# Performance work log

Hardware: AMD Instinct MI355X
Metric: run time of the kernel (lower is better)

Reference implementation:

```python
import jax, jax.numpy as jnp
import numpy as np

NUM_POSITIONS = 4096
EMBED_DIM = 512
BSZ, SEQ_LEN = 16, 4096


def setup_inputs() -> dict:
    key = jax.random.key(0)
    k1, k2 = jax.random.split(key)
    input_tensor = jax.random.normal(k1, (BSZ, SEQ_LEN, EMBED_DIM), dtype=jnp.float32)
    pv = jax.random.normal(k2, (NUM_POSITIONS, EMBED_DIM), dtype=jnp.float32)
    # L2-normalize each position vector (as in _init_position_vectors)
    pv = pv / jnp.linalg.norm(pv, axis=1, keepdims=True)
    return {"input_tensor": input_tensor, "position_vectors": pv}


def reference(input_tensor, position_vectors):
    # input_tensor: [B, S, D]; position_vectors: [P, D] with S <= P.
    seq_len, d = input_tensor.shape[1], input_tensor.shape[-1]
    pos = position_vectors[:seq_len]  # [S, D]
    # Batched circular convolution over the last axis via rFFT.
    x_fft = jnp.fft.rfft(input_tensor, axis=-1)          # [B, S, D//2+1] complex
    p_fft = jnp.fft.rfft(pos, axis=-1)[None, :, :]       # [1, S, D//2+1]
    out = jnp.fft.irfft(x_fft * p_fft, n=d, axis=-1)     # [B, S, D]
    return out.astype(input_tensor.dtype)
```

## Files before the change

kernel.cpp:

```cpp
#include <hip/hip_runtime.h>
#include <math.h>

#ifndef M_PI
#define M_PI 3.14159265358979323846
#endif

#define BSZ 16
#define SEQ 4096
#define DIM 512

#define REG_SZ 656

__device__ __forceinline__ float2 cadd(float2 a, float2 b){ return make_float2(a.x+b.x, a.y+b.y); }
__device__ __forceinline__ float2 csub(float2 a, float2 b){ return make_float2(a.x-b.x, a.y-b.y); }
__device__ __forceinline__ float2 cmul(float2 a, float2 b){
  return make_float2(fmaf(a.x, b.x, -(a.y*b.y)), fmaf(a.x, b.y, a.y*b.x));
}
__device__ __forceinline__ float2 cmulc(float2 a, float2 b){
  return make_float2(fmaf(a.x, b.x, a.y*b.y), fmaf(a.y, b.x, -(a.x*b.y)));
}
__device__ __forceinline__ float2 mul_mi(float2 a){ return make_float2(a.y, -a.x); }

__device__ __forceinline__ void dft8(const float2* in, float2* out){
  float2 t0 = cadd(in[0], in[4]), t1 = csub(in[0], in[4]);
  float2 t2 = cadd(in[2], in[6]), t3 = csub(in[2], in[6]);
  float2 E0 = cadd(t0, t2), E2 = csub(t0, t2);
  float2 m3 = mul_mi(t3);
  float2 E1 = cadd(t1, m3), E3 = csub(t1, m3);
  float2 s0 = cadd(in[1], in[5]), s1 = csub(in[1], in[5]);
  float2 s2 = cadd(in[3], in[7]), s3 = csub(in[3], in[7]);
  float2 O0 = cadd(s0, s2), O2 = csub(s0, s2);
  float2 n3 = mul_mi(s3);
  float2 O1 = cadd(s1, n3), O3 = csub(s1, n3);
  const float C = 0.70710678118654752440f;
  float2 w1o = make_float2(C*(O1.x + O1.y), C*(O1.y - O1.x));
  float2 w2o = mul_mi(O2);
  float2 w3o = make_float2(C*(O3.y - O3.x), -(C*(O3.x + O3.y)));
  out[0] = cadd(E0, O0); out[4] = csub(E0, O0);
  out[1] = cadd(E1, w1o); out[5] = csub(E1, w1o);
  out[2] = cadd(E2, w2o); out[6] = csub(E2, w2o);
  out[3] = cadd(E3, w3o); out[7] = csub(E3, w3o);
}

__device__ __forceinline__ void idft8(const float2* in, float2* out){
  float2 t[8];
  dft8(in, t);
  out[0]=t[0]; out[1]=t[7]; out[2]=t[6]; out[3]=t[5];
  out[4]=t[4]; out[5]=t[3]; out[6]=t[2]; out[7]=t[1];
}

__device__ __forceinline__ void fft512_fwd(float2* v, float2* lds, int lane,
                                           const float2* wA, const float2* wB){
  const int a = lane >> 3, b = lane & 7;
  float2 t[8];
  dft8(v, t);
  #pragma unroll
  for (int r = 1; r < 8; ++r) t[r] = cmul(t[r], wA[r]);
  __syncthreads();
  #pragma unroll
  for (int r = 0; r < 8; ++r) lds[72*r + lane] = t[r];
  __syncthreads();
  #pragma unroll
  for (int j2 = 0; j2 < 8; ++j2) v[j2] = lds[72*a + b + 8*j2];
  dft8(v, t);
  #pragma unroll
  for (int r2 = 1; r2 < 8; ++r2) t[r2] = cmul(t[r2], wB[r2]);
  __syncthreads();
  #pragma unroll
  for (int r2 = 0; r2 < 8; ++r2) lds[a + 82*r2 + 10*b] = t[r2];
  __syncthreads();
  #pragma unroll
  for (int i2 = 0; i2 < 8; ++i2) v[i2] = lds[a + 82*b + 10*i2];
  dft8(v, t);
  #pragma unroll
  for (int m = 0; m < 8; ++m) v[m] = t[m];
}

__device__ __forceinline__ void fft512_inv(float2* v, float2* lds, int lane,
                                           const float2* wA, const float2* wB){
  const int a = lane >> 3, b = lane & 7;
  float2 t[8];
  idft8(v, t);
  __syncthreads();
  #pragma unroll
  for (int i2 = 0; i2 < 8; ++i2) lds[a + 82*b + 10*i2] = t[i2];
  __syncthreads();
  #pragma unroll
  for (int r2 = 0; r2 < 8; ++r2) v[r2] = lds[a + 82*r2 + 10*b];
  #pragma unroll
  for (int r2 = 1; r2 < 8; ++r2) v[r2] = cmulc(v[r2], wB[r2]);
  idft8(v, t);
  __syncthreads();
  #pragma unroll
  for (int j2 = 0; j2 < 8; ++j2) lds[72*a + b + 8*j2] = t[j2];
  __syncthreads();
  #pragma unroll
  for (int r = 0; r < 8; ++r) v[r] = lds[72*r + lane];
  #pragma unroll
  for (int r = 1; r < 8; ++r) v[r] = cmulc(v[r], wA[r]);
  idft8(v, t);
  #pragma unroll
  for (int j = 0; j < 8; ++j) v[j] = t[j];
}

__global__ void __launch_bounds__(256)
circconv_kernel(const float* __restrict__ x, const float* __restrict__ p,
                float* __restrict__ out){
  __shared__ float2 lds_all[4 * REG_SZ];
  const int lane = threadIdx.x & 63;
  const int wid  = threadIdx.x >> 6;
  float2* lds = lds_all + wid * REG_SZ;

  const int g    = blockIdx.x * 4 + wid;
  const int s    = g >> 1;
  const int half = g & 1;
  const int b    = lane & 7;

  float2 wA[8], wB[8];
  wA[0] = make_float2(1.f, 0.f); wB[0] = make_float2(1.f, 0.f);
  #pragma unroll
  for (int r = 1; r < 8; ++r){
    float sv, cv;
    sincosf(-2.0f*(float)M_PI*(float)(lane*r)*(1.0f/512.0f), &sv, &cv);
    wA[r] = make_float2(cv, sv);
    sincosf(-2.0f*(float)M_PI*(float)(b*r)*(1.0f/64.0f), &sv, &cv);
    wB[r] = make_float2(cv, sv);
  }

  float2 pf[8];
  {
    const float* prow = p + (size_t)s * DIM;
    #pragma unroll
    for (int j = 0; j < 8; ++j) pf[j] = make_float2(prow[lane + 64*j], 0.f);
    fft512_fwd(pf, lds, lane, wA, wB);
    #pragma unroll
    for (int m = 0; m < 8; ++m){ pf[m].x *= (1.0f/512.0f); pf[m].y *= (1.0f/512.0f); }
  }

  const int b_lo = half * 8;
  for (int bb = b_lo; bb < b_lo + 8; bb += 2){
    const size_t base0 = ((size_t)bb       * SEQ + s) * DIM;
    const size_t base1 = ((size_t)(bb + 1) * SEQ + s) * DIM;
    float2 v[8];
    #pragma unroll
    for (int j = 0; j < 8; ++j)
      v[j] = make_float2(x[base0 + lane + 64*j], x[base1 + lane + 64*j]);
    fft512_fwd(v, lds, lane, wA, wB);
    #pragma unroll
    for (int m = 0; m < 8; ++m) v[m] = cmul(v[m], pf[m]);
    fft512_inv(v, lds, lane, wA, wB);
    #pragma unroll
    for (int j = 0; j < 8; ++j){
      out[base0 + lane + 64*j] = v[j].x;
      out[base1 + lane + 64*j] = v[j].y;
    }
  }
}

extern "C" void kernel_launch(void* const* d_in, const int* in_sizes, int n_in,
                              void* d_out, int out_size, void* d_ws, size_t ws_size,
                              hipStream_t stream) {
  (void)in_sizes; (void)n_in; (void)d_ws; (void)ws_size; (void)out_size;
  const float* x  = (const float*)d_in[0];
  const float* p  = (const float*)d_in[1];
  float* o        = (float*)d_out;
  circconv_kernel<<<SEQ*2/4, 256, 0, stream>>>(x, p, o);
}
```

Baseline: 245.1 us.

## Use wave-level LDS sync and prefetch next batch rows during FFT

Each wave owns a private LDS region, so the block-wide barriers are replaced with an lgkmcnt wait plus a wave barrier. The kernel also issues the loads for the position row and the first batch pair up front, then software-pipelines the batch loop by loading the next pair of rows into registers while the current pair goes through its FFTs. The aim is to remove inter-wave barrier stalls and hide global-load latency behind compute. The cost is higher register pressure from the prefetch buffers, which could reduce occupancy.

```diff
diff --git a/kernel.cpp b/kernel.cpp
--- a/kernel.cpp
+++ b/kernel.cpp
@@ -10,6 +10,11 @@
 #define DIM 512
 
 #define REG_SZ 656
+
+__device__ __forceinline__ void wsync(){
+  asm volatile("s_waitcnt lgkmcnt(0)" ::: "memory");
+  __builtin_amdgcn_wave_barrier();
+}
 
 __device__ __forceinline__ float2 cadd(float2 a, float2 b){ return make_float2(a.x+b.x, a.y+b.y); }
 __device__ __forceinline__ float2 csub(float2 a, float2 b){ return make_float2(a.x-b.x, a.y-b.y); }
@@ -56,19 +61,19 @@
   dft8(v, t);
   #pragma unroll
   for (int r = 1; r < 8; ++r) t[r] = cmul(t[r], wA[r]);
-  __syncthreads();
+  wsync();
   #pragma unroll
   for (int r = 0; r < 8; ++r) lds[72*r + lane] = t[r];
-  __syncthreads();
+  wsync();
   #pragma unroll
   for (int j2 = 0; j2 < 8; ++j2) v[j2] = lds[72*a + b + 8*j2];
   dft8(v, t);
   #pragma unroll
   for (int r2 = 1; r2 < 8; ++r2) t[r2] = cmul(t[r2], wB[r2]);
-  __syncthreads();
+  wsync();
   #pragma unroll
   for (int r2 = 0; r2 < 8; ++r2) lds[a + 82*r2 + 10*b] = t[r2];
-  __syncthreads();
+  wsync();
   #pragma unroll
   for (int i2 = 0; i2 < 8; ++i2) v[i2] = lds[a + 82*b + 10*i2];
   dft8(v, t);
@@ -81,19 +86,19 @@
   const int a = lane >> 3, b = lane & 7;
   float2 t[8];
   idft8(v, t);
-  __syncthreads();
+  wsync();
   #pragma unroll
   for (int i2 = 0; i2 < 8; ++i2) lds[a + 82*b + 10*i2] = t[i2];
-  __syncthreads();
+  wsync();
   #pragma unroll
   for (int r2 = 0; r2 < 8; ++r2) v[r2] = lds[a + 82*r2 + 10*b];
   #pragma unroll
   for (int r2 = 1; r2 < 8; ++r2) v[r2] = cmulc(v[r2], wB[r2]);
   idft8(v, t);
-  __syncthreads();
+  wsync();
   #pragma unroll
   for (int j2 = 0; j2 < 8; ++j2) lds[72*a + b + 8*j2] = t[j2];
-  __syncthreads();
+  wsync();
   #pragma unroll
   for (int r = 0; r < 8; ++r) v[r] = lds[72*r + lane];
   #pragma unroll
@@ -116,6 +121,24 @@
   const int half = g & 1;
   const int b    = lane & 7;
 
+  float pr[8];
+  {
+    const float* prow = p + (size_t)s * DIM;
+    #pragma unroll
+    for (int j = 0; j < 8; ++j) pr[j] = prow[lane + 64*j];
+  }
+
+  const int b_lo = half * 8;
+  const size_t row_stride = (size_t)SEQ * DIM;
+  size_t pf_base0 = ((size_t)b_lo * SEQ + s) * DIM;
+  size_t pf_base1 = pf_base0 + row_stride;
+  float r0[8], r1[8];
+  #pragma unroll
+  for (int j = 0; j < 8; ++j){
+    r0[j] = x[pf_base0 + lane + 64*j];
+    r1[j] = x[pf_base1 + lane + 64*j];
+  }
+
   float2 wA[8], wB[8];
   wA[0] = make_float2(1.f, 0.f); wB[0] = make_float2(1.f, 0.f);
   #pragma unroll
@@ -128,31 +151,38 @@
   }
 
   float2 pf[8];
-  {
-    const float* prow = p + (size_t)s * DIM;
-    #pragma unroll
-    for (int j = 0; j < 8; ++j) pf[j] = make_float2(prow[lane + 64*j], 0.f);
-    fft512_fwd(pf, lds, lane, wA, wB);
-    #pragma unroll
-    for (int m = 0; m < 8; ++m){ pf[m].x *= (1.0f/512.0f); pf[m].y *= (1.0f/512.0f); }
-  }
+  #pragma unroll
+  for (int j = 0; j < 8; ++j) pf[j] = make_float2(pr[j], 0.f);
+  fft512_fwd(pf, lds, lane, wA, wB);
+  #pragma unroll
+  for (int m = 0; m < 8; ++m){ pf[m].x *= (1.0f/512.0f); pf[m].y *= (1.0f/512.0f); }
 
-  const int b_lo = half * 8;
-  for (int bb = b_lo; bb < b_lo + 8; bb += 2){
-    const size_t base0 = ((size_t)bb       * SEQ + s) * DIM;
-    const size_t base1 = ((size_t)(bb + 1) * SEQ + s) * DIM;
+  for (int pi = 0; pi < 4; ++pi){
+    const size_t cb0 = ((size_t)(b_lo + 2*pi) * SEQ + s) * DIM;
+    const size_t cb1 = cb0 + row_stride;
+
     float2 v[8];
     #pragma unroll
-    for (int j = 0; j < 8; ++j)
-      v[j] = make_float2(x[base0 + lane + 64*j], x[base1 + lane + 64*j]);
+    for (int j = 0; j < 8; ++j) v[j] = make_float2(r0[j], r1[j]);
+
+    if (pi < 3){
+      const size_t nb0 = cb0 + 2*row_stride;
+      const size_t nb1 = nb0 + row_stride;
+      #pragma unroll
+      for (int j = 0; j < 8; ++j){
+        r0[j] = x[nb0 + lane + 64*j];
+        r1[j] = x[nb1 + lane + 64*j];
+      }
+    }
+
     fft512_fwd(v, lds, lane, wA, wB);
     #pragma unroll
     for (int m = 0; m < 8; ++m) v[m] = cmul(v[m], pf[m]);
     fft512_inv(v, lds, lane, wA, wB);
     #pragma unroll
     for (int j = 0; j < 8; ++j){
-      out[base0 + lane + 64*j] = v[j].x;
-      out[base1 + lane + 64*j] = v[j].y;
+      out[cb0 + lane + 64*j] = v[j].x;
+      out[cb1 + lane + 64*j] = v[j].y;
     }
   }
 }
```

After: 248.1 us. No clear change (+1.2%).
